# Kernel tuning notes

Hardware: AMD Instinct MI355X
Metric: run time of the kernel (lower is better)

Reference implementation:

```python
import jax, jax.numpy as jnp
import numpy as np
from jax import lax

OBS_LEN = 8
PRED_LEN = 12
BATCH = 131072
EMB = 128
HID = 128


def _lstm_cell(h, c, x, Wih, Whh, b):
    # PyTorch LSTM gate order: i, f, g, o
    z = x @ Wih + h @ Whh + b  # (B, 4H)
    i, f, g, o = jnp.split(z, 4, axis=-1)
    c_new = jax.nn.sigmoid(f) * c + jax.nn.sigmoid(i) * jnp.tanh(g)
    h_new = jax.nn.sigmoid(o) * jnp.tanh(c_new)
    return h_new, c_new


def setup_inputs() -> dict:
    key = jax.random.key(0)
    ks = jax.random.split(key, 8)
    p = lambda k, s: jax.random.normal(k, s, dtype=jnp.float32) * 0.1
    return {
        "obs_traj": jax.random.normal(ks[0], (OBS_LEN, BATCH, 2), dtype=jnp.float32),
        # encoder input embedding (Linear 2 -> EMB)
        "We": p(ks[1], (2, EMB)), "be": jnp.zeros((EMB,), jnp.float32),
        # encoder LSTM
        "Wih_e": p(ks[2], (EMB, 4 * HID)), "Whh_e": p(ks[3], (HID, 4 * HID)),
        "b_e": jnp.zeros((4 * HID,), jnp.float32),
        # decoder input embedding (Linear 2 -> EMB)
        "Wd": p(ks[4], (2, EMB)), "bd": jnp.zeros((EMB,), jnp.float32),
        # decoder LSTM
        "Wih_d": p(ks[5], (EMB, 4 * HID)), "Whh_d": p(ks[6], (HID, 4 * HID)),
        "b_d": jnp.zeros((4 * HID,), jnp.float32),
        # hidden2pos (Linear HID -> 2)
        "Wo": p(ks[7], (HID, 2)), "bo": jnp.zeros((2,), jnp.float32),
        "pred_len": PRED_LEN,
    }


def reference(obs_traj, We, be, Wih_e, Whh_e, b_e, Wd, bd, Wih_d, Whh_d, b_d, Wo, bo, pred_len):
    B = obs_traj.shape[1]
    H = Whh_e.shape[0]
    dt = obs_traj.dtype

    # ---- Encoder: embed positions, run LSTM over obs_len ----
    emb = obs_traj @ We + be  # (obs_len, B, EMB)
    h0 = jnp.zeros((B, H), dt)
    c0 = jnp.zeros((B, H), dt)

    def enc_step(carry, x_t):
        h, c = carry
        h, c = _lstm_cell(h, c, x_t, Wih_e, Whh_e, b_e)
        return (h, c), None

    (h_enc, _), _ = lax.scan(enc_step, (h0, c0), emb)

    # ---- Decoder: state = (h_final, zeros); first pos directly from h_final ----
    pos0 = h_enc @ Wo + bo  # (B, 2)
    h_d = h_enc
    c_d = jnp.zeros_like(h_enc)

    def dec_step(carry, _):
        h, c, pos = carry
        x = pos @ Wd + bd  # embed previous predicted position
        h, c = _lstm_cell(h, c, x, Wih_d, Whh_d, b_d)
        pos_new = h @ Wo + bo
        return (h, c, pos_new), pos_new

    _, rest = lax.scan(dec_step, (h_d, c_d, pos0), None, length=pred_len - 1)
    pred_traj = jnp.concatenate([pos0[None], rest], axis=0)  # (pred_len, B, 2)
    return pred_traj
```

## Files before the change

kernel.cpp:

```cpp
#include <hip/hip_runtime.h>


#define OBS_LEN 8
#define PRED_LEN 12
#define BATCH 131072
#define HID 128
#define NZ 512
#define KWT 128
#define CROWS 32
#define ROWSB 64

typedef float f32x4 __attribute__((ext_vector_type(4)));
typedef float f32x2 __attribute__((ext_vector_type(2)));
typedef unsigned short u16x8 __attribute__((ext_vector_type(8)));
typedef __bf16 bf16x8 __attribute__((ext_vector_type(8)));

#define K2F 1.4426950408889634f

static __device__ __forceinline__ unsigned short cvt1(float f) {
  __bf16 b = (__bf16)f;
  return __builtin_bit_cast(unsigned short, b);
}
static __device__ __forceinline__ float bf2f(unsigned short h) {
  return __uint_as_float(((unsigned int)h) << 16);
}

__global__ void prep_weights(const float* __restrict__ We,   const float* __restrict__ be,
                             const float* __restrict__ Wih_e,const float* __restrict__ Whh_e,
                             const float* __restrict__ b_e,
                             const float* __restrict__ Wd,   const float* __restrict__ bd,
                             const float* __restrict__ Wih_d,const float* __restrict__ Whh_d,
                             const float* __restrict__ b_d,
                             const float* __restrict__ Wo,   const float* __restrict__ bo,
                             unsigned short* __restrict__ wt_enc,
                             unsigned short* __restrict__ wt_dec,
                             float* __restrict__ aux_enc, float* __restrict__ aux_dec) {
  const int c = blockIdx.x & (NZ - 1);
  const bool dec = blockIdx.x >= NZ;
  const int cg = c >> 6, gate = (c >> 4) & 3, cl = c & 15;
  const int unit = cg * 16 + cl;
  const int n = gate * HID + unit;

  const float* Whh = dec ? Whh_d : Whh_e;
  const float* Wih = dec ? Wih_d : Wih_e;
  const float* Wem = dec ? Wd : We;
  const float* bem = dec ? bd : be;
  const float* bl  = dec ? b_d : b_e;
  unsigned short* wt = dec ? wt_dec : wt_enc;

  float wx = 0.f, wy = 0.f;
  for (int e = 0; e < HID; ++e) {
    wx += Wem[e] * Wih[e * NZ + n];
    wy += Wem[HID + e] * Wih[e * NZ + n];
  }
  for (int k = threadIdx.x; k < KWT; k += 64) {
    float v = Whh[k * NZ + n];
    if (dec) v += Wo[k * 2] * wx + Wo[k * 2 + 1] * wy;
    wt[c * KWT + k] = cvt1(v);
  }
  if (threadIdx.x == 0) {
    float bb = bl[n];
    for (int e = 0; e < HID; ++e) bb += bem[e] * Wih[e * NZ + n];
    if (!dec) {
      aux_enc[n] = wx; aux_enc[NZ + n] = wy; aux_enc[2 * NZ + n] = bb;
    } else {
      aux_dec[n] = bb + bo[0] * wx + bo[1] * wy;
    }
  }
}


#define EXP4(D, S)                                                             \
  { f32x4 _s = (S);                                                            \
    D[0] = __builtin_amdgcn_exp2f(_s[0]); D[1] = __builtin_amdgcn_exp2f(_s[1]);\
    D[2] = __builtin_amdgcn_exp2f(_s[2]); D[3] = __builtin_amdgcn_exp2f(_s[3]); }
#define RCP4(D, S)                                                             \
  { f32x4 _r = (S);                                                            \
    D[0] = __builtin_amdgcn_rcpf(_r[0]); D[1] = __builtin_amdgcn_rcpf(_r[1]);  \
    D[2] = __builtin_amdgcn_rcpf(_r[2]); D[3] = __builtin_amdgcn_rcpf(_r[3]); }

#define LOADW(WB)                                                              \
  { _Pragma("unroll")                                                          \
    for (int kc = 0; kc < 4; ++kc) {                                           \
      _Pragma("unroll")                                                        \
      for (int nt = 0; nt < 4; ++nt)                                           \
        bfr[kc][nt] = *(const u16x8*)((WB) + nt * 16 * KWT + kc * 32);         \
    } }

#define INITC(ACC, BB)                                                         \
  { _Pragma("unroll")                                                          \
    for (int m = 0; m < 2; ++m) {                                              \
      _Pragma("unroll")                                                        \
      for (int g = 0; g < 4; ++g)                                              \
        ACC[m][g] = (f32x4){(BB)[g], (BB)[g], (BB)[g], (BB)[g]};               \
    } }

#define MMSTEP(ACC, HB, BB)                                                    \
  { INITC(ACC, BB)                                                             \
    _Pragma("unroll")                                                          \
    for (int kc = 0; kc < 4; ++kc) {                                           \
      const int _g = (((kc * 4 + l4) ^ (l15 & 7)) << 3);                       \
      u16x8 _a0 = *(const u16x8*)&hL[HB][l15 * 128 + _g];                      \
      u16x8 _a1 = *(const u16x8*)&hL[HB][(16 + l15) * 128 + _g];               \
      _Pragma("unroll")                                                        \
      for (int g = 0; g < 4; ++g) {                                            \
        ACC[0][g] = __builtin_amdgcn_mfma_f32_16x16x32_bf16(                   \
            __builtin_bit_cast(bf16x8, _a0),                                   \
            __builtin_bit_cast(bf16x8, bfr[kc][g]), ACC[0][g], 0, 0, 0);       \
        ACC[1][g] = __builtin_amdgcn_mfma_f32_16x16x32_bf16(                   \
            __builtin_bit_cast(bf16x8, _a1),                                   \
            __builtin_bit_cast(bf16x8, bfr[kc][g]), ACC[1][g], 0, 0, 0);       \
      } } }

#define GATEC(ACC, CRR, HB, FOLD)                                              \
  { _Pragma("unroll")                                                          \
    for (int m = 0; m < 2; ++m) {                                              \
      f32x4 g_zi = ACC[m][0], g_zf = ACC[m][1];                                \
      f32x4 g_zg = ACC[m][2], g_zo = ACC[m][3];                                \
      if (FOLD) {                                                              \
        f32x4 g_px = m ? px1 : px0, g_py = m ? py1 : py0;                      \
        g_zi += g_px * wx[0] + g_py * wy[0];                                   \
        g_zf += g_px * wx[1] + g_py * wy[1];                                   \
        g_zg += g_px * wx[2] + g_py * wy[2];                                   \
        g_zo += g_px * wx[3] + g_py * wy[3];                                   \
      }                                                                        \
      f32x4 g_eB, g_eA, g_eG, g_eO;                                            \
      EXP4(g_eB, g_zi * (-K2F)) EXP4(g_eA, g_zf * (-K2F))                      \
      EXP4(g_eG, g_zg * (-2.f * K2F)) EXP4(g_eO, g_zo * (-K2F))                \
      f32x4 g_a1 = 1.f + g_eA, g_b1 = 1.f + g_eB, g_g1 = 1.f + g_eG;           \
      f32x4 g_bg = g_b1 * g_g1;                                                \
      f32x4 g_rd; RCP4(g_rd, g_a1 * g_bg)                                      \
      f32x4 g_cv = (CRR[m] * g_bg + (1.f - g_eG) * g_a1) * g_rd;               \
      CRR[m] = g_cv;                                                           \
      f32x4 g_eC; EXP4(g_eC, g_cv * (-2.f * K2F))                              \
      f32x4 g_rh; RCP4(g_rh, (1.f + g_eO) * (1.f + g_eC))                      \
      f32x4 g_hv = (1.f - g_eC) * g_rh;                                        \
      const int g_R0 = 16 * m + l4 * 4;                                        \
      _Pragma("unroll")                                                        \
      for (int r = 0; r < 4; ++r)                                              \
        hL[HB][(g_R0 + r) * 128 + ((uh ^ ((g_R0 + r) & 7)) << 3) + ul] =       \
            cvt1(g_hv[r]);                                                     \
    } }

#define POSC(S, HB, CO)                                                        \
  { const int pp_r = tid >> 4, pp_q = tid & 15;                                \
    u16x8 pp_h =                                                               \
        *(const u16x8*)&hL[HB][pp_r * 128 + ((pp_q ^ (pp_r & 7)) << 3)];       \
    const float* pp_w = Wo + pp_q * 16;                                        \
    f32x4 pp_w0 = *(const f32x4*)pp_w;                                         \
    f32x4 pp_w1 = *(const f32x4*)(pp_w + 4);                                   \
    f32x4 pp_w2 = *(const f32x4*)(pp_w + 8);                                   \
    f32x4 pp_w3 = *(const f32x4*)(pp_w + 12);                                  \
    f32x2 pp_s = (f32x2){0.f, 0.f};                                            \
    pp_s += bf2f(pp_h[0]) * (f32x2){pp_w0[0], pp_w0[1]};                       \
    pp_s += bf2f(pp_h[1]) * (f32x2){pp_w0[2], pp_w0[3]};                       \
    pp_s += bf2f(pp_h[2]) * (f32x2){pp_w1[0], pp_w1[1]};                       \
    pp_s += bf2f(pp_h[3]) * (f32x2){pp_w1[2], pp_w1[3]};                       \
    pp_s += bf2f(pp_h[4]) * (f32x2){pp_w2[0], pp_w2[1]};                       \
    pp_s += bf2f(pp_h[5]) * (f32x2){pp_w2[2], pp_w2[3]};                       \
    pp_s += bf2f(pp_h[6]) * (f32x2){pp_w3[0], pp_w3[1]};                       \
    pp_s += bf2f(pp_h[7]) * (f32x2){pp_w3[2], pp_w3[3]};                       \
    pp_s[0] += __shfl_xor(pp_s[0], 1); pp_s[1] += __shfl_xor(pp_s[1], 1);      \
    pp_s[0] += __shfl_xor(pp_s[0], 2); pp_s[1] += __shfl_xor(pp_s[1], 2);      \
    pp_s[0] += __shfl_xor(pp_s[0], 4); pp_s[1] += __shfl_xor(pp_s[1], 4);      \
    pp_s[0] += __shfl_xor(pp_s[0], 8); pp_s[1] += __shfl_xor(pp_s[1], 8);      \
    if (pp_q == 0) {                                                           \
      float2 pp_o; pp_o.x = pp_s[0] + bo0; pp_o.y = pp_s[1] + bo1;             \
      ((float2*)out)[(size_t)(S)*BATCH + row0 + (CO) + pp_r] = pp_o;           \
    } }

#define LOADP(T, CO)                                                           \
  { const float* lp_b =                                                        \
        obs + 2 * ((size_t)(T)*BATCH + row0 + (CO) + l4 * 4);                  \
    f32x4 lp_q0 = *(const f32x4*)lp_b;                                         \
    f32x4 lp_q1 = *(const f32x4*)(lp_b + 4);                                   \
    f32x4 lp_q2 = *(const f32x4*)(lp_b + 32);                                  \
    f32x4 lp_q3 = *(const f32x4*)(lp_b + 36);                                  \
    px0 = (f32x4){lp_q0[0], lp_q0[2], lp_q1[0], lp_q1[2]};                     \
    py0 = (f32x4){lp_q0[1], lp_q0[3], lp_q1[1], lp_q1[3]};                     \
    px1 = (f32x4){lp_q2[0], lp_q2[2], lp_q3[0], lp_q3[2]};                     \
    py1 = (f32x4){lp_q2[1], lp_q2[3], lp_q3[1], lp_q3[3]}; }

__global__ __launch_bounds__(512, 2) void lstm_fused(
    const float* __restrict__ obs,
    const unsigned short* __restrict__ wt_enc,
    const unsigned short* __restrict__ wt_dec,
    const float* __restrict__ aux_enc, const float* __restrict__ aux_dec,
    const float* __restrict__ Wo, const float* __restrict__ bo,
    float* __restrict__ out) {
  __shared__ unsigned short hL[2][CROWS * 128];

  const int tid = threadIdx.x;
  const int lane = tid & 63;
  const int cg = tid >> 6;
  const int l15 = lane & 15;
  const int l4 = lane >> 4;
  const int row0 = blockIdx.x * ROWSB;
  const int u = cg * 16 + l15;
  const int uh = u >> 3, ul = u & 7;

  const float bo0 = bo[0], bo1 = bo[1];

  const unsigned short* wBe = wt_enc + (cg * 64 + l15) * KWT + l4 * 8;
  const unsigned short* wBd = wt_dec + (cg * 64 + l15) * KWT + l4 * 8;

  u16x8 bfr[4][4];
  LOADW(wBe);

  float wx[4], wy[4], bbE[4], bbD[4];
#pragma unroll
  for (int g = 0; g < 4; ++g) {
    wx[g]  = aux_enc[g * HID + u];
    wy[g]  = aux_enc[NZ + g * HID + u];
    bbE[g] = aux_enc[2 * NZ + g * HID + u];
  }

  f32x4 accA[2][4], accB[2][4];
  f32x4 crrA[2], crrB[2];
  crrA[0] = crrA[1] = (f32x4){0.f, 0.f, 0.f, 0.f};
  crrB[0] = crrB[1] = (f32x4){0.f, 0.f, 0.f, 0.f};
  f32x4 px0, py0, px1, py1;

  LOADP(0, 0)
  INITC(accA, bbE)
  GATEC(accA, crrA, 0, 1)
  __syncthreads();

  LOADP(0, CROWS)
  MMSTEP(accA, 0, bbE)
  INITC(accB, bbE)
  GATEC(accB, crrB, 1, 1)
  __syncthreads();

  LOADP(1, 0)
  MMSTEP(accB, 1, bbE)
  GATEC(accA, crrA, 0, 1)
  __syncthreads();

#pragma unroll 1
  for (int t = 2; t < OBS_LEN; ++t) {
    LOADP(t - 1, CROWS)
    MMSTEP(accA, 0, bbE)
    GATEC(accB, crrB, 1, 1)
    __syncthreads();
    LOADP(t, 0)
    MMSTEP(accB, 1, bbE)
    GATEC(accA, crrA, 0, 1)
    __syncthreads();
  }

  LOADW(wBd);
#pragma unroll
  for (int g = 0; g < 4; ++g) bbD[g] = aux_dec[g * HID + u];
  crrA[0] = crrA[1] = (f32x4){0.f, 0.f, 0.f, 0.f};

  LOADP(OBS_LEN - 1, CROWS)
  MMSTEP(accA, 0, bbD)
  GATEC(accB, crrB, 1, 1)
  POSC(0, 0, 0)
  __syncthreads();
  crrB[0] = crrB[1] = (f32x4){0.f, 0.f, 0.f, 0.f};

  MMSTEP(accB, 1, bbD)
  GATEC(accA, crrA, 0, 0)
  POSC(0, 1, CROWS)
  __syncthreads();

#pragma unroll 1
  for (int d = 2; d < PRED_LEN; ++d) {
    MMSTEP(accA, 0, bbD)
    GATEC(accB, crrB, 1, 0)
    POSC(d - 1, 0, 0)
    __syncthreads();
    MMSTEP(accB, 1, bbD)
    GATEC(accA, crrA, 0, 0)
    POSC(d - 1, 1, CROWS)
    __syncthreads();
  }

  GATEC(accB, crrB, 1, 0)
  POSC(PRED_LEN - 1, 0, 0)
  __syncthreads();
  POSC(PRED_LEN - 1, 1, CROWS)
}

extern "C" void kernel_launch(void* const* d_in, const int* in_sizes, int n_in,
                              void* d_out, int out_size, void* d_ws, size_t ws_size,
                              hipStream_t stream) {
  const float* obs   = (const float*)d_in[0];
  const float* We    = (const float*)d_in[1];
  const float* be    = (const float*)d_in[2];
  const float* Wih_e = (const float*)d_in[3];
  const float* Whh_e = (const float*)d_in[4];
  const float* b_e   = (const float*)d_in[5];
  const float* Wd    = (const float*)d_in[6];
  const float* bd    = (const float*)d_in[7];
  const float* Wih_d = (const float*)d_in[8];
  const float* Whh_d = (const float*)d_in[9];
  const float* b_d   = (const float*)d_in[10];
  const float* Wo    = (const float*)d_in[11];
  const float* bo    = (const float*)d_in[12];
  float* out = (float*)d_out;

  unsigned short* wt_enc = (unsigned short*)d_ws;
  unsigned short* wt_dec = wt_enc + NZ * KWT;
  float* aux_enc = (float*)(wt_dec + NZ * KWT);
  float* aux_dec = aux_enc + 3 * NZ;

  hipLaunchKernelGGL(prep_weights, dim3(2 * NZ), dim3(64), 0, stream,
                     We, be, Wih_e, Whh_e, b_e, Wd, bd, Wih_d, Whh_d, b_d,
                     Wo, bo, wt_enc, wt_dec, aux_enc, aux_dec);
  hipLaunchKernelGGL(lstm_fused, dim3(BATCH / ROWSB), dim3(512), 0, stream,
                     obs, wt_enc, wt_dec, aux_enc, aux_dec, Wo, bo, out);
}
```

Baseline: 529.1 us.

## Split block into MFMA and gate warp groups with weights staged in LDS

Blocks grow to 1024 threads, split into two sides of eight waves. The side waves take turns: one runs the recurrent matmul while the other runs the gate nonlinearities, position loads and output projection, instead of each wave doing both in sequence. The recurrent weights move from per-thread registers into a swizzled 128 KB LDS buffer that all waves read. This frees registers and specialises the waves, but adds LDS traffic on every MFMA step. The large LDS footprint limits occupancy to one block per CU, and half the waves sit idle at any moment.

```diff
diff --git a/kernel.cpp b/kernel.cpp
--- a/kernel.cpp
+++ b/kernel.cpp
@@ -7,8 +7,6 @@
 #define HID 128
 #define NZ 512
 #define KWT 128
-#define CROWS 32
-#define ROWSB 64
 
 typedef float f32x4 __attribute__((ext_vector_type(4)));
 typedef float f32x2 __attribute__((ext_vector_type(2)));
@@ -79,44 +77,38 @@
     D[0] = __builtin_amdgcn_rcpf(_r[0]); D[1] = __builtin_amdgcn_rcpf(_r[1]);  \
     D[2] = __builtin_amdgcn_rcpf(_r[2]); D[3] = __builtin_amdgcn_rcpf(_r[3]); }
 
-#define LOADW(WB)                                                              \
-  { _Pragma("unroll")                                                          \
-    for (int kc = 0; kc < 4; ++kc) {                                           \
-      _Pragma("unroll")                                                        \
-      for (int nt = 0; nt < 4; ++nt)                                           \
-        bfr[kc][nt] = *(const u16x8*)((WB) + nt * 16 * KWT + kc * 32);         \
-    } }
-
-#define INITC(ACC, BB)                                                         \
+#define INITC()                                                                \
   { _Pragma("unroll")                                                          \
     for (int m = 0; m < 2; ++m) {                                              \
       _Pragma("unroll")                                                        \
       for (int g = 0; g < 4; ++g)                                              \
-        ACC[m][g] = (f32x4){(BB)[g], (BB)[g], (BB)[g], (BB)[g]};               \
+        acc[m][g] = (f32x4){bb[g], bb[g], bb[g], bb[g]};                       \
     } }
 
-#define MMSTEP(ACC, HB, BB)                                                    \
-  { INITC(ACC, BB)                                                             \
+#define MMLDS()                                                                \
+  { INITC()                                                                    \
     _Pragma("unroll")                                                          \
     for (int kc = 0; kc < 4; ++kc) {                                           \
-      const int _g = (((kc * 4 + l4) ^ (l15 & 7)) << 3);                       \
-      u16x8 _a0 = *(const u16x8*)&hL[HB][l15 * 128 + _g];                      \
-      u16x8 _a1 = *(const u16x8*)&hL[HB][(16 + l15) * 128 + _g];               \
+      const int gsh = (((kc * 4 + l4) ^ (l15 & 7)) << 3);                      \
+      u16x8 _a0 = *(const u16x8*)&Al[abase + l15 * 128 + gsh];                 \
+      u16x8 _a1 = *(const u16x8*)&Al[abase + (16 + l15) * 128 + gsh];          \
       _Pragma("unroll")                                                        \
-      for (int g = 0; g < 4; ++g) {                                            \
-        ACC[0][g] = __builtin_amdgcn_mfma_f32_16x16x32_bf16(                   \
-            __builtin_bit_cast(bf16x8, _a0),                                   \
-            __builtin_bit_cast(bf16x8, bfr[kc][g]), ACC[0][g], 0, 0, 0);       \
-        ACC[1][g] = __builtin_amdgcn_mfma_f32_16x16x32_bf16(                   \
-            __builtin_bit_cast(bf16x8, _a1),                                   \
-            __builtin_bit_cast(bf16x8, bfr[kc][g]), ACC[1][g], 0, 0, 0);       \
+      for (int nt = 0; nt < 4; ++nt) {                                         \
+        u16x8 _bf =                                                            \
+            *(const u16x8*)&Bl[(cg * 64 + nt * 16 + l15) * 128 + gsh];         \
+        acc[0][nt] = __builtin_amdgcn_mfma_f32_16x16x32_bf16(                  \
+            __builtin_bit_cast(bf16x8, _a0), __builtin_bit_cast(bf16x8, _bf),  \
+            acc[0][nt], 0, 0, 0);                                              \
+        acc[1][nt] = __builtin_amdgcn_mfma_f32_16x16x32_bf16(                  \
+            __builtin_bit_cast(bf16x8, _a1), __builtin_bit_cast(bf16x8, _bf),  \
+            acc[1][nt], 0, 0, 0);                                              \
       } } }
 
-#define GATEC(ACC, CRR, HB, FOLD)                                              \
+#define GATEC(FOLD)                                                            \
   { _Pragma("unroll")                                                          \
     for (int m = 0; m < 2; ++m) {                                              \
-      f32x4 g_zi = ACC[m][0], g_zf = ACC[m][1];                                \
-      f32x4 g_zg = ACC[m][2], g_zo = ACC[m][3];                                \
+      f32x4 g_zi = acc[m][0], g_zf = acc[m][1];                                \
+      f32x4 g_zg = acc[m][2], g_zo = acc[m][3];                                \
       if (FOLD) {                                                              \
         f32x4 g_px = m ? px1 : px0, g_py = m ? py1 : py0;                      \
         g_zi += g_px * wx[0] + g_py * wy[0];                                   \
@@ -130,23 +122,23 @@
       f32x4 g_a1 = 1.f + g_eA, g_b1 = 1.f + g_eB, g_g1 = 1.f + g_eG;           \
       f32x4 g_bg = g_b1 * g_g1;                                                \
       f32x4 g_rd; RCP4(g_rd, g_a1 * g_bg)                                      \
-      f32x4 g_cv = (CRR[m] * g_bg + (1.f - g_eG) * g_a1) * g_rd;               \
-      CRR[m] = g_cv;                                                           \
+      f32x4 g_cv = (crr[m] * g_bg + (1.f - g_eG) * g_a1) * g_rd;               \
+      crr[m] = g_cv;                                                           \
       f32x4 g_eC; EXP4(g_eC, g_cv * (-2.f * K2F))                              \
       f32x4 g_rh; RCP4(g_rh, (1.f + g_eO) * (1.f + g_eC))                      \
       f32x4 g_hv = (1.f - g_eC) * g_rh;                                        \
       const int g_R0 = 16 * m + l4 * 4;                                        \
       _Pragma("unroll")                                                        \
       for (int r = 0; r < 4; ++r)                                              \
-        hL[HB][(g_R0 + r) * 128 + ((uh ^ ((g_R0 + r) & 7)) << 3) + ul] =       \
+        Al[abase + (g_R0 + r) * 128 + ((uh ^ ((g_R0 + r) & 7)) << 3) + ul] =   \
             cvt1(g_hv[r]);                                                     \
     } }
 
-#define POSC(S, HB, CO)                                                        \
-  { const int pp_r = tid >> 4, pp_q = tid & 15;                                \
-    u16x8 pp_h =                                                               \
-        *(const u16x8*)&hL[HB][pp_r * 128 + ((pp_q ^ (pp_r & 7)) << 3)];       \
-    const float* pp_w = Wo + pp_q * 16;                                        \
+#define POSC(S, CH)                                                            \
+  { const int pp_r = st >> 4, pp_q = st & 15;                                  \
+    u16x8 pp_h = *(const u16x8*)&Al[(CH)*4096 + pp_r * 128 +                   \
+                                    ((pp_q ^ (pp_r & 7)) << 3)];               \
+    const float* pp_w = WoL + pp_q * 16;                                       \
     f32x4 pp_w0 = *(const f32x4*)pp_w;                                         \
     f32x4 pp_w1 = *(const f32x4*)(pp_w + 4);                                   \
     f32x4 pp_w2 = *(const f32x4*)(pp_w + 8);                                   \
@@ -166,12 +158,12 @@
     pp_s[0] += __shfl_xor(pp_s[0], 8); pp_s[1] += __shfl_xor(pp_s[1], 8);      \
     if (pp_q == 0) {                                                           \
       float2 pp_o; pp_o.x = pp_s[0] + bo0; pp_o.y = pp_s[1] + bo1;             \
-      ((float2*)out)[(size_t)(S)*BATCH + row0 + (CO) + pp_r] = pp_o;           \
+      ((float2*)out)[(size_t)(S)*BATCH + row0 + (CH)*32 + pp_r] = pp_o;        \
     } }
 
-#define LOADP(T, CO)                                                           \
+#define LOADP(T)                                                               \
   { const float* lp_b =                                                        \
-        obs + 2 * ((size_t)(T)*BATCH + row0 + (CO) + l4 * 4);                  \
+        obs + 2 * ((size_t)(T)*BATCH + row0 + side * 32 + l4 * 4);             \
     f32x4 lp_q0 = *(const f32x4*)lp_b;                                         \
     f32x4 lp_q1 = *(const f32x4*)(lp_b + 4);                                   \
     f32x4 lp_q2 = *(const f32x4*)(lp_b + 32);                                  \
@@ -181,107 +173,105 @@
     px1 = (f32x4){lp_q2[0], lp_q2[2], lp_q3[0], lp_q3[2]};                     \
     py1 = (f32x4){lp_q2[1], lp_q2[3], lp_q3[1], lp_q3[3]}; }
 
-__global__ __launch_bounds__(512, 2) void lstm_fused(
+#define SMEM_BYTES (((NZ * 128) + (2 * 32 * 128)) * 2 + 128 * 2 * 4)
+
+__global__ __launch_bounds__(1024, 1) void lstm_fused(
     const float* __restrict__ obs,
     const unsigned short* __restrict__ wt_enc,
     const unsigned short* __restrict__ wt_dec,
     const float* __restrict__ aux_enc, const float* __restrict__ aux_dec,
     const float* __restrict__ Wo, const float* __restrict__ bo,
     float* __restrict__ out) {
-  __shared__ unsigned short hL[2][CROWS * 128];
+  extern __shared__ unsigned short smem_u16[];
+  unsigned short* Bl = smem_u16;
+  unsigned short* Al = smem_u16 + NZ * 128;
+  float* WoL = (float*)(smem_u16 + NZ * 128 + 2 * 32 * 128);
 
   const int tid = threadIdx.x;
   const int lane = tid & 63;
-  const int cg = tid >> 6;
+  const int wn = tid >> 6;
+  const int side = wn >> 3;
+  const int cg = wn & 7;
+  const int st = tid & 511;
   const int l15 = lane & 15;
   const int l4 = lane >> 4;
-  const int row0 = blockIdx.x * ROWSB;
-  const int u = cg * 16 + l15;
-  const int uh = u >> 3, ul = u & 7;
-
+  const int row0 = blockIdx.x * 64;
+  const int u = cg * 16 + l15, uh = u >> 3, ul = u & 7;
+  const int abase = side * 4096;
   const float bo0 = bo[0], bo1 = bo[1];
 
-  const unsigned short* wBe = wt_enc + (cg * 64 + l15) * KWT + l4 * 8;
-  const unsigned short* wBd = wt_dec + (cg * 64 + l15) * KWT + l4 * 8;
-
-  u16x8 bfr[4][4];
-  LOADW(wBe);
-
-  float wx[4], wy[4], bbE[4], bbD[4];
+  {
+    const int sc = wn * 32 + (lane >> 1);
+    const unsigned short* ssrc = wt_enc + sc * KWT + (lane & 1) * 64;
+    unsigned short* sdst = Bl + sc * 128;
+#pragma unroll
+    for (int j = 0; j < 8; ++j) {
+      const int gw = (lane & 1) * 8 + j;
+      *(u16x8*)&sdst[(gw ^ (sc & 7)) << 3] = *(const u16x8*)(ssrc + j * 8);
+    }
+  }
+  *(u16x8*)&Al[tid * 8] = (u16x8){0, 0, 0, 0, 0, 0, 0, 0};
+  if (tid < HID) { WoL[tid * 2] = Wo[tid * 2]; WoL[tid * 2 + 1] = Wo[tid * 2 + 1]; }
+
+  float wx[4], wy[4], bb[4];
 #pragma unroll
   for (int g = 0; g < 4; ++g) {
-    wx[g]  = aux_enc[g * HID + u];
-    wy[g]  = aux_enc[NZ + g * HID + u];
-    bbE[g] = aux_enc[2 * NZ + g * HID + u];
-  }
-
-  f32x4 accA[2][4], accB[2][4];
-  f32x4 crrA[2], crrB[2];
-  crrA[0] = crrA[1] = (f32x4){0.f, 0.f, 0.f, 0.f};
-  crrB[0] = crrB[1] = (f32x4){0.f, 0.f, 0.f, 0.f};
+    wx[g] = aux_enc[g * HID + u];
+    wy[g] = aux_enc[NZ + g * HID + u];
+    bb[g] = aux_enc[2 * NZ + g * HID + u];
+  }
+
+  f32x4 acc[2][4];
+  f32x4 crr[2];
+  crr[0] = crr[1] = (f32x4){0.f, 0.f, 0.f, 0.f};
   f32x4 px0, py0, px1, py1;
-
-  LOADP(0, 0)
-  INITC(accA, bbE)
-  GATEC(accA, crrA, 0, 1)
-  __syncthreads();
-
-  LOADP(0, CROWS)
-  MMSTEP(accA, 0, bbE)
-  INITC(accB, bbE)
-  GATEC(accB, crrB, 1, 1)
-  __syncthreads();
-
-  LOADP(1, 0)
-  MMSTEP(accB, 1, bbE)
-  GATEC(accA, crrA, 0, 1)
   __syncthreads();
 
 #pragma unroll 1
-  for (int t = 2; t < OBS_LEN; ++t) {
-    LOADP(t - 1, CROWS)
-    MMSTEP(accA, 0, bbE)
-    GATEC(accB, crrB, 1, 1)
+  for (int t = 0; t < OBS_LEN; ++t) {
+    if (side == 0) { MMLDS() }
+    else if (t > 0) { LOADP(t - 1) GATEC(1) }
     __syncthreads();
-    LOADP(t, 0)
-    MMSTEP(accB, 1, bbE)
-    GATEC(accA, crrA, 0, 1)
+    if (side == 1) { MMLDS() }
+    else { LOADP(t) GATEC(1) }
     __syncthreads();
   }
 
-  LOADW(wBd);
+  if (side == 0) {
+    const int dc = cg * 64 + lane;
+    const unsigned short* dsrc = wt_dec + dc * KWT;
+    unsigned short* ddst = Bl + dc * 128;
 #pragma unroll
-  for (int g = 0; g < 4; ++g) bbD[g] = aux_dec[g * HID + u];
-  crrA[0] = crrA[1] = (f32x4){0.f, 0.f, 0.f, 0.f};
-
-  LOADP(OBS_LEN - 1, CROWS)
-  MMSTEP(accA, 0, bbD)
-  GATEC(accB, crrB, 1, 1)
-  POSC(0, 0, 0)
-  __syncthreads();
-  crrB[0] = crrB[1] = (f32x4){0.f, 0.f, 0.f, 0.f};
-
-  MMSTEP(accB, 1, bbD)
-  GATEC(accA, crrA, 0, 0)
-  POSC(0, 1, CROWS)
+    for (int j = 0; j < 16; ++j)
+      *(u16x8*)&ddst[(j ^ (dc & 7)) << 3] = *(const u16x8*)(dsrc + j * 8);
+  } else {
+    LOADP(OBS_LEN - 1) GATEC(1)
+  }
+  crr[0] = crr[1] = (f32x4){0.f, 0.f, 0.f, 0.f};
+#pragma unroll
+  for (int g = 0; g < 4; ++g) bb[g] = aux_dec[g * HID + u];
+  __syncthreads();
+
+  if (side == 0) { MMLDS() }
+  else { POSC(0, 0) }
+  __syncthreads();
+  if (side == 1) { MMLDS() }
+  else { GATEC(0) POSC(0, 1) }
   __syncthreads();
 
 #pragma unroll 1
   for (int d = 2; d < PRED_LEN; ++d) {
-    MMSTEP(accA, 0, bbD)
-    GATEC(accB, crrB, 1, 0)
-    POSC(d - 1, 0, 0)
+    if (side == 0) { MMLDS() }
+    else { GATEC(0) POSC(d - 1, 0) }
     __syncthreads();
-    MMSTEP(accB, 1, bbD)
-    GATEC(accA, crrA, 0, 0)
-    POSC(d - 1, 1, CROWS)
+    if (side == 1) { MMLDS() }
+    else { GATEC(0) POSC(d - 1, 1) }
     __syncthreads();
   }
 
-  GATEC(accB, crrB, 1, 0)
-  POSC(PRED_LEN - 1, 0, 0)
-  __syncthreads();
-  POSC(PRED_LEN - 1, 1, CROWS)
+  if (side == 1) { GATEC(0) POSC(PRED_LEN - 1, 0) }
+  __syncthreads();
+  if (side == 0) { POSC(PRED_LEN - 1, 1) }
 }
 
 extern "C" void kernel_launch(void* const* d_in, const int* in_sizes, int n_in,
@@ -307,9 +297,12 @@
   float* aux_enc = (float*)(wt_dec + NZ * KWT);
   float* aux_dec = aux_enc + 3 * NZ;
 
+  hipFuncSetAttribute((const void*)lstm_fused,
+                      hipFuncAttributeMaxDynamicSharedMemorySize, SMEM_BYTES);
+
   hipLaunchKernelGGL(prep_weights, dim3(2 * NZ), dim3(64), 0, stream,
                      We, be, Wih_e, Whh_e, b_e, Wd, bd, Wih_d, Whh_d, b_d,
                      Wo, bo, wt_enc, wt_dec, aux_enc, aux_dec);
-  hipLaunchKernelGGL(lstm_fused, dim3(BATCH / ROWSB), dim3(512), 0, stream,
-                     obs, wt_enc, wt_dec, aux_enc, aux_dec, Wo, bo, out);
-}
+  hipLaunchKernelGGL(lstm_fused, dim3(BATCH / 64), dim3(1024), SMEM_BYTES,
+                     stream, obs, wt_enc, wt_dec, aux_enc, aux_dec, Wo, bo, out);
+}
```

New measurement: 774.4 us. +46.4%, slower.
